# Optimization experiments

Hardware: AMD Instinct MI355X
Metric: run time of the kernel (lower is better)

Reference implementation:

```python
import jax, jax.numpy as jnp
import numpy as np

D_MODEL = 1024
HEADS = 16
D_K = D_MODEL // HEADS
THETA = 10000.0
NEG = -1.0e9


def _rope(t, offset=0):
    # t: [B, H, S, D]; standard interleaved rotary embedding, base THETA
    S, D = t.shape[-2], t.shape[-1]
    half = D // 2
    inv_freq = 1.0 / (THETA ** (jnp.arange(half, dtype=jnp.float32) * 2.0 / D))
    pos = jnp.arange(offset, offset + S, dtype=jnp.float32)
    ang = pos[:, None] * inv_freq[None, :]          # [S, half]
    cos, sin = jnp.cos(ang), jnp.sin(ang)
    t1, t2 = t[..., ::2], t[..., 1::2]              # even / odd lanes
    o1 = t1 * cos - t2 * sin
    o2 = t1 * sin + t2 * cos
    return jnp.stack([o1, o2], axis=-1).reshape(t.shape)


def setup_inputs() -> dict:
    key = jax.random.key(0)
    k0, k1, k2, k3, k4 = jax.random.split(key, 5)
    B, S = 2, 2048
    x = jax.random.normal(k0, (B, S, D_MODEL), dtype=jnp.float32)
    att_mask = jnp.ones((B, S), dtype=jnp.int32)
    scale = 0.02
    wq = jax.random.normal(k1, (D_MODEL, D_MODEL), dtype=jnp.float32) * scale
    wk = jax.random.normal(k2, (D_MODEL, D_MODEL), dtype=jnp.float32) * scale
    wv = jax.random.normal(k3, (D_MODEL, D_MODEL), dtype=jnp.float32) * scale
    wo = jax.random.normal(k4, (D_MODEL, D_MODEL), dtype=jnp.float32) * scale
    return {"x": x, "att_mask": att_mask, "wq": wq, "wk": wk, "wv": wv, "wo": wo}


def reference(x, att_mask, wq, wk, wv, wo):
    B, S, _ = x.shape
    # nn.Linear(bias=False): y = x @ W^T ; then split heads -> [B, H, S, d_k]
    q = (x @ wq.T).reshape(B, S, HEADS, D_K).transpose(0, 2, 1, 3)
    k = (x @ wk.T).reshape(B, S, HEADS, D_K).transpose(0, 2, 1, 3)
    v = (x @ wv.T).reshape(B, S, HEADS, D_K).transpose(0, 2, 1, 3)
    # use_rope=True, start_pos=0, use_cache=False path
    q = _rope(q)
    k = _rope(k)
    scores = jnp.einsum("bhqd,bhkd->bhqk", q, k) / np.sqrt(D_K).astype(np.float32)
    pad = (att_mask == 0)[:, None, None, :]          # [B,1,1,S]
    scores = jnp.where(pad, NEG, scores)
    causal = jnp.tril(jnp.ones((S, S), dtype=bool))  # [S, S]
    scores = jnp.where(causal, scores, NEG)
    att = jax.nn.softmax(scores, axis=-1)
    ctx = jnp.einsum("bhqk,bhkd->bhqd", att, v)      # [B,H,S,d_k]
    final = ctx.transpose(0, 2, 1, 3).reshape(B, S, HEADS * D_K)
    return final @ wo.T
```

## Files before the change

### kernel.cpp

```cpp
#include <hip/hip_runtime.h>
#include <hip/hip_bf16.h>
#include <cstdint>

typedef unsigned short u16;
typedef __bf16 bf16x8 __attribute__((ext_vector_type(8)));
typedef float f32x4 __attribute__((ext_vector_type(4)));

#define S_LEN 2048
#define NH 16
#define DK 64
#define DM 1024

__device__ __forceinline__ u16 f2bf(float f) {
  union { float f; uint32_t u; } c; c.f = f;
  uint32_t u = c.u;
  u += 0x7fffu + ((u >> 16) & 1u);
  return (u16)(u >> 16);
}

__device__ __forceinline__ void gl_lds16(const void* gsrc, void* ldst) {
  __builtin_amdgcn_global_load_lds(
      (const __attribute__((address_space(1))) unsigned int*)gsrc,
      (__attribute__((address_space(3))) unsigned int*)ldst,
      16, 0, 0);
}

#define MFMA16(a, b, c) __builtin_amdgcn_mfma_f32_16x16x32_bf16((a), (b), (c), 0, 0, 0)
#define VMW(N) asm volatile("s_waitcnt vmcnt(" #N ")" ::: "memory")
#define BARM() asm volatile("s_barrier" ::: "memory")

__global__ __launch_bounds__(256) void prep_all(
    const float* x, const float* wq, const float* wk, const float* wv, const float* wo,
    const int* amask,
    u16* xb, u16* wqb, u16* wkb, u16* wvb, u16* wob, float2* tab, int* mflag)
{
  const int bid = blockIdx.x;
  if (bid < 2048) {
#pragma unroll
    for (int it = 0; it < 4; ++it) {
      size_t i = ((size_t)bid * 256 + threadIdx.x) * 4 + (size_t)it * 2097152u;
      const float* src; u16* dst; size_t off;
      if (i < 4194304u)      { src = x;  dst = xb;  off = i; }
      else if (i < 5242880u) { src = wq; dst = wqb; off = i - 4194304u; }
      else if (i < 6291456u) { src = wk; dst = wkb; off = i - 5242880u; }
      else if (i < 7340032u) { src = wv; dst = wvb; off = i - 6291456u; }
      else                   { src = wo; dst = wob; off = i - 7340032u; }
      float4 v = *(const float4*)(src + off);
      ushort4 o;
      o.x = f2bf(v.x); o.y = f2bf(v.y); o.z = f2bf(v.z); o.w = f2bf(v.w);
      *(ushort4*)(dst + off) = o;
    }
  } else if (bid < 2304) {
    int i = (bid - 2048) * 256 + threadIdx.x;
    int pos = i >> 5, f = i & 31;
    float inv = powf(10000.0f, -(float)f / 32.0f);
    float ang = (float)pos * inv;
    tab[i] = make_float2(cosf(ang), sinf(ang));
  } else {
    const int f = bid - 2304;
    if (threadIdx.x < 64) {
      const int b = f >> 5, t = f & 31;
      int v = amask[b * S_LEN + t * 64 + threadIdx.x];
      int all = (int)__all(v != 0);
      if (threadIdx.x == 0) mflag[f] = all;
    }
  }
}

__global__ __launch_bounds__(256, 4) void gemm_qkv32(
    const u16* xb, const u16* wqb, const u16* wkb, const u16* wvb,
    const float2* tab, u16* Qr, u16* Kr, u16* Vt)
{
  __shared__ __align__(16) u16 ldsA[2][128 * 32];
  __shared__ __align__(16) u16 ldsB[2][128 * 32];

  const int bid = blockIdx.x;
  const int xcd = bid & 7, v = bid >> 3;
  const int m0 = (xcd * 4 + (v & 3)) * 128;
  const int nc = v >> 2;
  const int z = nc >> 3;
  const int n0z = (nc & 7) * 128;
  const u16* Wz = (z == 0) ? wqb : ((z == 1) ? wkb : wvb);

  const int tid = threadIdx.x;
  const int w = tid >> 6, lane = tid & 63;
  const int l15 = lane & 15, g = lane >> 4;
  const int wm = (w >> 1) * 64, wn = (w & 1) * 64;
  const int lr4 = lane >> 2;
  const int scolb = ((lane & 3) * 16) ^ ((lr4 & 3) << 4);

  f32x4 acc[4][4] = {};

  auto stage = [&](int buf, int kt) {
#pragma unroll
    for (int c = 0; c < 2; ++c) {
      const int rb = c * 64 + w * 16;
      const int row = rb + lr4;
      gl_lds16((const char*)(xb + (size_t)(m0 + row) * DM + kt) + scolb,
               (char*)&ldsA[buf][0] + rb * 64);
      gl_lds16((const char*)(Wz + (size_t)(n0z + row) * DM + kt) + scolb,
               (char*)&ldsB[buf][0] + rb * 64);
    }
  };

  stage(0, 0);
  int cur = 0;
  for (int kt = 0; kt < DM; kt += 32) {
    if (kt + 32 < DM) { stage(cur ^ 1, kt + 32); VMW(4); } else { VMW(0); }
    BARM();
    bf16x8 af[4], bfr[4];
#pragma unroll
    for (int i = 0; i < 4; ++i) {
      const int ar = wm + i * 16 + l15;
      af[i] = *(const bf16x8*)((const char*)&ldsA[cur][0] + ar * 64 +
                               ((g * 16) ^ ((ar & 3) << 4)));
      const int br = wn + i * 16 + l15;
      bfr[i] = *(const bf16x8*)((const char*)&ldsB[cur][0] + br * 64 +
                                ((g * 16) ^ ((br & 3) << 4)));
    }
    __builtin_amdgcn_s_setprio(1);
#pragma unroll
    for (int i = 0; i < 4; ++i)
#pragma unroll
      for (int j = 0; j < 4; ++j)
        acc[i][j] = MFMA16(af[i], bfr[j], acc[i][j]);
    __builtin_amdgcn_s_setprio(0);
    BARM();
    cur ^= 1;
  }

  u16* dst = (z == 0) ? Qr : Kr;
#pragma unroll
  for (int i = 0; i < 4; ++i) {
#pragma unroll
    for (int j = 0; j < 4; ++j) {
      const int n = n0z + wn + j * 16 + l15;
      const int h = n >> 6, d = n & 63;
#pragma unroll
      for (int r = 0; r < 4; ++r) {
        const int m = m0 + wm + i * 16 + g * 4 + r;
        const int b = m >> 11, s = m & 2047;
        float vv = acc[i][j][r];
        if (z < 2) {
          float p = __shfl_xor(vv, 1);
          float2 cs = tab[s * 32 + (d >> 1)];
          float o = vv * cs.x + ((d & 1) ? p : -p) * cs.y;
          if (z == 0) o *= 0.18033688011f;
          dst[((size_t)(b * NH + h) * S_LEN + s) * DK + d] = f2bf(o);
        } else {
          Vt[((size_t)(b * NH + h) * DK + d) * S_LEN + s] = f2bf(vv);
        }
      }
    }
  }
}

__global__ __launch_bounds__(256, 4) void gemm_out64(const u16* ctx, const u16* wob, float* out) {
  __shared__ __align__(16) u16 ldsA[2][128 * 32];
  __shared__ __align__(16) u16 ldsB[2][64 * 32];

  const int bid = blockIdx.x;
  const int xcd = bid & 7, v = bid >> 3;
  const int m0 = (xcd * 4 + (v & 3)) * 128;
  const int n0 = (v >> 2) * 64;

  const int tid = threadIdx.x;
  const int w = tid >> 6, lane = tid & 63;
  const int l15 = lane & 15, g = lane >> 4;
  const int wm = (w >> 1) * 64, wn = (w & 1) * 32;
  const int lr4 = lane >> 2;
  const int scolb = ((lane & 3) * 16) ^ ((lr4 & 3) << 4);

  f32x4 acc[4][2] = {};

  auto stage = [&](int buf, int kt) {
#pragma unroll
    for (int c = 0; c < 2; ++c) {
      const int rb = c * 64 + w * 16;
      const int row = rb + lr4;
      gl_lds16((const char*)(ctx + (size_t)(m0 + row) * DM + kt) + scolb,
               (char*)&ldsA[buf][0] + rb * 64);
    }
    const int rb = w * 16;
    const int row = rb + lr4;
    gl_lds16((const char*)(wob + (size_t)(n0 + row) * DM + kt) + scolb,
             (char*)&ldsB[buf][0] + rb * 64);
  };

  stage(0, 0);
  int cur = 0;
  for (int kt = 0; kt < DM; kt += 32) {
    if (kt + 32 < DM) { stage(cur ^ 1, kt + 32); VMW(3); } else { VMW(0); }
    BARM();
    bf16x8 af[4], bfr[2];
#pragma unroll
    for (int i = 0; i < 4; ++i) {
      const int ar = wm + i * 16 + l15;
      af[i] = *(const bf16x8*)((const char*)&ldsA[cur][0] + ar * 64 +
                               ((g * 16) ^ ((ar & 3) << 4)));
    }
#pragma unroll
    for (int j = 0; j < 2; ++j) {
      const int br = wn + j * 16 + l15;
      bfr[j] = *(const bf16x8*)((const char*)&ldsB[cur][0] + br * 64 +
                                ((g * 16) ^ ((br & 3) << 4)));
    }
    __builtin_amdgcn_s_setprio(1);
#pragma unroll
    for (int i = 0; i < 4; ++i)
#pragma unroll
      for (int j = 0; j < 2; ++j)
        acc[i][j] = MFMA16(af[i], bfr[j], acc[i][j]);
    __builtin_amdgcn_s_setprio(0);
    BARM();
    cur ^= 1;
  }

#pragma unroll
  for (int i = 0; i < 4; ++i)
#pragma unroll
    for (int j = 0; j < 2; ++j)
#pragma unroll
      for (int r = 0; r < 4; ++r)
        out[(size_t)(m0 + wm + i * 16 + g * 4 + r) * DM + n0 + wn + j * 16 + l15] = acc[i][j][r];
}

__global__ __launch_bounds__(512, 4) void attn11(
    const u16* Qr, const u16* Kr, const u16* Vt, const int* amask, const int* mflag,
    u16* ctx)
{
  __shared__ __align__(16) u16 ldsK[2][64 * 64];
  __shared__ __align__(16) u16 ldsV[2][64 * 64];
  __shared__ __align__(16) __bf16 plds[8][16 * 72];

  const int bh = blockIdx.x;
  const int by = blockIdx.y;
  const int band = (by < 8) ? (15 - by) : (by - 8);
  const int b = bh >> 4, h = bh & 15;
  const int tid = threadIdx.x, w8 = tid >> 6, lane = tid & 63;
  const int l15 = lane & 15, g = lane >> 4;
  const int r8 = lane >> 3;
  const int sw = ((lane & 7) * 16) ^ (r8 << 4);

  const int chunk = band * 4 + (w8 >> 1);
  const int q0 = chunk * 32 + (w8 & 1) * 16;
  const int myNt = (chunk >> 1) + 1;
  const int dTile = chunk >> 1;
  const int ntB = band * 2 + 2;

  const u16* Kb0 = Kr + (size_t)bh * S_LEN * DK;
  const u16* Vb0 = Vt + (size_t)bh * DK * S_LEN;
  const u16* Qb  = Qr + (size_t)bh * S_LEN * DK;

  bf16x8 qa0 = *(const bf16x8*)(Qb + (size_t)(q0 + l15) * DK + g * 8);
  bf16x8 qa1 = *(const bf16x8*)(Qb + (size_t)(q0 + l15) * DK + 32 + g * 8);

  union { u16 u[8]; bf16x8 v; } one_u;
#pragma unroll
  for (int i = 0; i < 8; ++i) one_u.u[i] = 0x3F80;
  const bf16x8 ones = one_u.v;

  float m[4];
  f32x4 lacc = {0.f, 0.f, 0.f, 0.f};
  f32x4 o[4];
#pragma unroll
  for (int r = 0; r < 4; ++r) m[r] = -3e38f;
#pragma unroll
  for (int dt = 0; dt < 4; ++dt) o[dt] = (f32x4){0.f, 0.f, 0.f, 0.f};

  auto stage = [&](int buf, int t) {
    const size_t kv0 = (size_t)t * 64;
    const int row = w8 * 8 + r8;
    gl_lds16((const char*)(Kb0 + (kv0 + row) * DK) + sw,
             (char*)&ldsK[buf][0] + (w8 * 8) * 128);
    gl_lds16((const char*)(Vb0 + (size_t)row * S_LEN + kv0) + sw,
             (char*)&ldsV[buf][0] + (w8 * 8) * 128);
  };

  stage(0, 0);
  int cur = 0;

  for (int t = 0; t < ntB; ++t) {
    if (t + 1 < ntB) { stage(cur ^ 1, t + 1); VMW(2); } else { VMW(0); }
    BARM();
    if (t < myNt) {
      const int kv0 = t * 64;
      const bool allok = mflag[(b << 5) + t] != 0;

      bf16x8 kb[4][2];
#pragma unroll
      for (int nt = 0; nt < 4; ++nt) {
        const int row = nt * 16 + l15;
#pragma unroll
        for (int ks = 0; ks < 2; ++ks)
          kb[nt][ks] = *(const bf16x8*)((const char*)&ldsK[cur][0] + row * 128 +
                                        ((ks * 64 + g * 16) ^ ((row & 7) << 4)));
      }
      f32x4 s[4];
#pragma unroll
      for (int nt = 0; nt < 4; ++nt) s[nt] = (f32x4){0.f, 0.f, 0.f, 0.f};
      __builtin_amdgcn_s_setprio(1);
#pragma unroll
      for (int nt = 0; nt < 4; ++nt) {
        s[nt] = MFMA16(qa0, kb[nt][0], s[nt]);
        s[nt] = MFMA16(qa1, kb[nt][1], s[nt]);
      }
      __builtin_amdgcn_s_setprio(0);

      if (!allok) {
#pragma unroll
        for (int nt = 0; nt < 4; ++nt) {
          const int pmv = amask[b * S_LEN + kv0 + nt * 16 + l15];
#pragma unroll
          for (int r = 0; r < 4; ++r)
            if (!pmv) s[nt][r] = -1e9f;
        }
      }
      if (t == dTile) {
#pragma unroll
        for (int nt = 0; nt < 4; ++nt) {
          const int kvc = kv0 + nt * 16 + l15;
#pragma unroll
          for (int r = 0; r < 4; ++r)
            s[nt][r] = (kvc <= q0 + g * 4 + r) ? s[nt][r] : -1e9f;
        }
      }

      float tmax[4];
      bool need = false;
#pragma unroll
      for (int r = 0; r < 4; ++r) {
        float t0 = fmaxf(fmaxf(s[0][r], s[1][r]), fmaxf(s[2][r], s[3][r]));
        t0 = fmaxf(t0, __shfl_xor(t0, 1));
        t0 = fmaxf(t0, __shfl_xor(t0, 2));
        t0 = fmaxf(t0, __shfl_xor(t0, 4));
        t0 = fmaxf(t0, __shfl_xor(t0, 8));
        tmax[r] = t0;
        need = need || (t0 > m[r] + 11.5415603f);
      }
      if (__any((int)need)) {
#pragma unroll
        for (int r = 0; r < 4; ++r) {
          const float mnew = fmaxf(m[r], tmax[r]);
          const float alpha = exp2f(m[r] - mnew);
          m[r] = mnew;
          lacc[r] *= alpha;
#pragma unroll
          for (int dt = 0; dt < 4; ++dt) o[dt][r] *= alpha;
        }
      }
      __bf16* pw = &plds[w8][0];
#pragma unroll
      for (int r = 0; r < 4; ++r) {
#pragma unroll
        for (int nt = 0; nt < 4; ++nt)
          pw[(g * 4 + r) * 72 + nt * 16 + l15] = (__bf16)exp2f(s[nt][r] - m[r]);
      }
      bf16x8 pa0 = *(const bf16x8*)(pw + l15 * 72 + g * 8);
      bf16x8 pa1 = *(const bf16x8*)(pw + l15 * 72 + 32 + g * 8);
      bf16x8 vb[4][2];
#pragma unroll
      for (int dt = 0; dt < 4; ++dt) {
        const int row = dt * 16 + l15;
#pragma unroll
        for (int ks = 0; ks < 2; ++ks)
          vb[dt][ks] = *(const bf16x8*)((const char*)&ldsV[cur][0] + row * 128 +
                                        ((ks * 64 + g * 16) ^ ((row & 7) << 4)));
      }
      __builtin_amdgcn_s_setprio(1);
      lacc = MFMA16(pa0, ones, lacc);
      lacc = MFMA16(pa1, ones, lacc);
#pragma unroll
      for (int dt = 0; dt < 4; ++dt) {
        o[dt] = MFMA16(pa0, vb[dt][0], o[dt]);
        o[dt] = MFMA16(pa1, vb[dt][1], o[dt]);
      }
      __builtin_amdgcn_s_setprio(0);
    }
    BARM();
    cur ^= 1;
  }

#pragma unroll
  for (int dt = 0; dt < 4; ++dt)
#pragma unroll
    for (int r = 0; r < 4; ++r) {
      const int q = q0 + g * 4 + r;
      ctx[((size_t)(b * S_LEN + q)) * DM + h * DK + dt * 16 + l15] =
          f2bf(o[dt][r] / lacc[r]);
    }
}

extern "C" void kernel_launch(void* const* d_in, const int* in_sizes, int n_in,
                              void* d_out, int out_size, void* d_ws, size_t ws_size,
                              hipStream_t stream) {
  const float* x   = (const float*)d_in[0];
  const int* amask = (const int*)d_in[1];
  const float* wq  = (const float*)d_in[2];
  const float* wk  = (const float*)d_in[3];
  const float* wv  = (const float*)d_in[4];
  const float* wo  = (const float*)d_in[5];
  float* out = (float*)d_out;

  char* ws = (char*)d_ws;
  u16* xb    = (u16*)(ws);
  u16* wqb   = (u16*)(ws + ( 8u << 20));
  u16* wkb   = (u16*)(ws + (10u << 20));
  u16* wvb   = (u16*)(ws + (12u << 20));
  u16* wob   = (u16*)(ws + (14u << 20));
  float2* tab = (float2*)(ws + (16u << 20));
  int* mflag = (int*)(ws + (16u << 20) + (768u << 10));
  u16* Qr    = (u16*)(ws + (17u << 20));
  u16* Kr    = (u16*)(ws + (25u << 20));
  u16* Vt    = (u16*)(ws + (33u << 20));
  u16* ctx   = (u16*)(ws + (41u << 20));

  hipLaunchKernelGGL(prep_all, dim3(2368), dim3(256), 0, stream,
                     x, wq, wk, wv, wo, amask, xb, wqb, wkb, wvb, wob, tab, mflag);
  hipLaunchKernelGGL(gemm_qkv32, dim3(768), dim3(256), 0, stream,
                     xb, wqb, wkb, wvb, tab, Qr, Kr, Vt);
  hipLaunchKernelGGL(attn11, dim3(32, 16), dim3(512), 0, stream,
                     Qr, Kr, Vt, amask, mflag, ctx);
  hipLaunchKernelGGL(gemm_out64, dim3(512), dim3(256), 0, stream, ctx, wob, out);
}
```

Baseline: 144.2 us.

## Split long causal attention bands across two blocks and merge partials

```diff
diff --git a/kernel.cpp b/kernel.cpp
--- a/kernel.cpp
+++ b/kernel.cpp
@@ -16,6 +16,11 @@
   uint32_t u = c.u;
   u += 0x7fffu + ((u >> 16) & 1u);
   return (u16)(u >> 16);
+}
+
+__device__ __forceinline__ float bf2f(u16 v) {
+  union { uint32_t u; float f; } c; c.u = ((uint32_t)v) << 16;
+  return c.f;
 }
 
 __device__ __forceinline__ void gl_lds16(const void* gsrc, void* ldst) {
@@ -225,17 +230,21 @@
         out[(size_t)(m0 + wm + i * 16 + g * 4 + r) * DM + n0 + wn + j * 16 + l15] = acc[i][j][r];
 }
 
-__global__ __launch_bounds__(512, 4) void attn11(
+__global__ __launch_bounds__(512, 6) void attn12(
     const u16* Qr, const u16* Kr, const u16* Vt, const int* amask, const int* mflag,
-    u16* ctx)
+    u16* ctx, u16* opart, float2* mlpart)
 {
   __shared__ __align__(16) u16 ldsK[2][64 * 64];
   __shared__ __align__(16) u16 ldsV[2][64 * 64];
   __shared__ __align__(16) __bf16 plds[8][16 * 72];
 
   const int bh = blockIdx.x;
-  const int by = blockIdx.y;
-  const int band = (by < 8) ? (15 - by) : (by - 8);
+  const int y = blockIdx.y;
+  const int j = y / 3, k = y % 3;
+  const int band = (k == 2) ? (7 - j) : (15 - j);
+  const int tLo  = (k == 1) ? (band + 1) : 0;
+  const int tEnd = (k == 0) ? (band + 1) : (2 * band + 2);
+
   const int b = bh >> 4, h = bh & 15;
   const int tid = threadIdx.x, w8 = tid >> 6, lane = tid & 63;
   const int l15 = lane & 15, g = lane >> 4;
@@ -246,7 +255,6 @@
   const int q0 = chunk * 32 + (w8 & 1) * 16;
   const int myNt = (chunk >> 1) + 1;
   const int dTile = chunk >> 1;
-  const int ntB = band * 2 + 2;
 
   const u16* Kb0 = Kr + (size_t)bh * S_LEN * DK;
   const u16* Vb0 = Vt + (size_t)bh * DK * S_LEN;
@@ -277,11 +285,11 @@
              (char*)&ldsV[buf][0] + (w8 * 8) * 128);
   };
 
-  stage(0, 0);
+  stage(0, tLo);
   int cur = 0;
 
-  for (int t = 0; t < ntB; ++t) {
-    if (t + 1 < ntB) { stage(cur ^ 1, t + 1); VMW(2); } else { VMW(0); }
+  for (int t = tLo; t < tEnd; ++t) {
+    if (t + 1 < tEnd) { stage(cur ^ 1, t + 1); VMW(2); } else { VMW(0); }
     BARM();
     if (t < myNt) {
       const int kv0 = t * 64;
@@ -381,14 +389,49 @@
     cur ^= 1;
   }
 
-#pragma unroll
-  for (int dt = 0; dt < 4; ++dt)
-#pragma unroll
-    for (int r = 0; r < 4; ++r) {
-      const int q = q0 + g * 4 + r;
-      ctx[((size_t)(b * S_LEN + q)) * DM + h * DK + dt * 16 + l15] =
-          f2bf(o[dt][r] / lacc[r]);
-    }
+  if (k == 2) {
+#pragma unroll
+    for (int dt = 0; dt < 4; ++dt)
+#pragma unroll
+      for (int r = 0; r < 4; ++r) {
+        const int q = q0 + g * 4 + r;
+        ctx[((size_t)(b * S_LEN + q)) * DM + h * DK + dt * 16 + l15] =
+            f2bf(o[dt][r] / lacc[r]);
+      }
+  } else {
+    const int prow0 = (bh * 8 + (band - 8)) * 128 + (q0 - band * 128);
+    u16* op = opart + (size_t)k * 32768 * 64;
+#pragma unroll
+    for (int dt = 0; dt < 4; ++dt)
+#pragma unroll
+      for (int r = 0; r < 4; ++r)
+        op[(size_t)(prow0 + g * 4 + r) * 64 + dt * 16 + l15] = f2bf(o[dt][r]);
+    if (l15 == 0) {
+#pragma unroll
+      for (int r = 0; r < 4; ++r)
+        mlpart[k * 32768 + prow0 + g * 4 + r] = make_float2(m[r], lacc[r]);
+    }
+  }
+}
+
+__global__ __launch_bounds__(256) void combine8(
+    const u16* opart, const float2* mlpart, u16* ctx)
+{
+  const int row = blockIdx.x * 4 + (threadIdx.x >> 6);
+  const int lane = threadIdx.x & 63;
+  float2 a = mlpart[row];
+  float2 c = mlpart[32768 + row];
+  float mm = fmaxf(a.x, c.x);
+  float w0 = exp2f(a.x - mm), w1 = exp2f(c.x - mm);
+  float l = a.y * w0 + c.y * w1;
+  float v0 = bf2f(opart[(size_t)row * 64 + lane]);
+  float v1 = bf2f(opart[(size_t)(32768 + row) * 64 + lane]);
+  float res = (v0 * w0 + v1 * w1) / l;
+  const int rr = row & 127, t2 = row >> 7;
+  const int boff = t2 & 7, bh = t2 >> 3;
+  const int q = (boff + 8) * 128 + rr;
+  const int b = bh >> 4, h = bh & 15;
+  ctx[((size_t)(b * S_LEN + q)) * DM + h * DK + lane] = f2bf(res);
 }
 
 extern "C" void kernel_launch(void* const* d_in, const int* in_sizes, int n_in,
@@ -415,11 +458,16 @@
   u16* Vt    = (u16*)(ws + (33u << 20));
   u16* ctx   = (u16*)(ws + (41u << 20));
 
+  u16* opart    = (u16*)(ws);
+  float2* mlpart = (float2*)(ws + (8u << 20));
+
   hipLaunchKernelGGL(prep_all, dim3(2368), dim3(256), 0, stream,
                      x, wq, wk, wv, wo, amask, xb, wqb, wkb, wvb, wob, tab, mflag);
   hipLaunchKernelGGL(gemm_qkv32, dim3(768), dim3(256), 0, stream,
                      xb, wqb, wkb, wvb, tab, Qr, Kr, Vt);
-  hipLaunchKernelGGL(attn11, dim3(32, 16), dim3(512), 0, stream,
-                     Qr, Kr, Vt, amask, mflag, ctx);
+  hipLaunchKernelGGL(attn12, dim3(32, 24), dim3(512), 0, stream,
+                     Qr, Kr, Vt, amask, mflag, ctx, opart, mlpart);
+  hipLaunchKernelGGL(combine8, dim3(8192), dim3(256), 0, stream,
+                     opart, mlpart, ctx);
   hipLaunchKernelGGL(gemm_out64, dim3(512), dim3(256), 0, stream, ctx, wob, out);
 }
```

Result: slower. 218.4 us (+51.4%).
